# Kernel optimization log

Measured on AMD Instinct MI355X. Metric: run time of the kernel, lower is better.

Reference implementation:

```python
import jax, jax.numpy as jnp
import numpy as np

B, L, D, F = 4096, 200, 64, 100000


def setup_inputs() -> dict:
    key = jax.random.key(0)
    ks = jax.random.split(key, 12)
    film_hist = jax.random.randint(ks[0], (B, L), 0, F)                 # padded rated-film indices
    ratings = jax.random.uniform(ks[1], (B, L), jnp.float32) * 4.5 + 0.5  # letterboxd-style 0.5..5
    lengths = jax.random.randint(ks[2], (B,), 1, L + 1)                 # ragged history lengths (>=1)
    film_indices = jax.random.randint(ks[3], (B,), 0, F)                # target films to score
    emb_table = jax.random.normal(ks[4], (F, D), jnp.float32) * 0.1
    W1 = jax.random.normal(ks[5], (5 * D, 2 * D), jnp.float32) * 0.05
    b1 = jnp.zeros((2 * D,), jnp.float32)
    W2 = jax.random.normal(ks[6], (2 * D, D), jnp.float32) * 0.05
    b2 = jnp.zeros((D,), jnp.float32)
    W3 = jax.random.normal(ks[7], (D, 1), jnp.float32) * 0.05
    b3 = jnp.zeros((1,), jnp.float32)
    return {"film_hist": film_hist, "ratings": ratings, "lengths": lengths,
            "film_indices": film_indices, "emb_table": emb_table,
            "W1": W1, "b1": b1, "W2": W2, "b2": b2, "W3": W3, "b3": b3}


def _user_embeddings(film_hist, ratings, lengths, emb_table):
    # mask[b, l] = l < lengths[b]
    mask = jnp.arange(L)[None, :] < lengths[:, None]          # [B, L]
    n = lengths.astype(jnp.float32)                           # [B]
    mean_r = jnp.sum(jnp.where(mask, ratings, 0.0), axis=1) / n
    weights = ratings - mean_r[:, None] + 0.1                 # [B, L]
    hist_emb = emb_table[film_hist]                           # [B, L, D]
    w = hist_emb * weights[:, :, None]                        # weighted film embeddings
    m3 = mask[:, :, None]
    wmin = jnp.min(jnp.where(m3, w, jnp.inf), axis=1)
    wmax = jnp.max(jnp.where(m3, w, -jnp.inf), axis=1)
    wmean = jnp.sum(jnp.where(m3, w, 0.0), axis=1) / n[:, None]
    # median: sort valid entries (pads go to +inf at the end); torch.median
    # returns the lower middle element -> index (n-1)//2
    ws = jnp.sort(jnp.where(m3, w, jnp.inf), axis=1)
    mid = ((lengths - 1) // 2)[:, None, None]                 # [B,1,1]
    wmed = jnp.take_along_axis(ws, jnp.broadcast_to(mid, (B, 1, D)), axis=1)[:, 0, :]
    ue = jnp.concatenate([wmin, wmax, wmean, wmed], axis=1)   # [B, 4D]
    return ue / jnp.linalg.norm(ue, axis=1, keepdims=True)


def reference(film_hist, ratings, lengths, film_indices, emb_table, W1, b1, W2, b2, W3, b3):
    ue = _user_embeddings(film_hist, ratings, lengths, emb_table)  # [B, 4D]
    fe = emb_table[film_indices]                                   # [B, D]
    x = jnp.concatenate([ue, fe], axis=1)                          # [B, 5D]
    h = jax.nn.relu(x @ W1 + b1)   # Dropout(0.2) is identity in eval
    h = jax.nn.relu(h @ W2 + b2)
    return jax.nn.sigmoid(h @ W3 + b3)[:, 0]                       # [B]
```

## Files before the change

### kernel.cpp

```cpp
#include <hip/hip_runtime.h>
#include <hip/hip_bf16.h>
#include <stdint.h>


#define B_ 4096
#define L_ 200
#define D_ 64

__global__ __launch_bounds__(256) void stats_kernel(
    const int* __restrict__ film_hist,
    const float* __restrict__ ratings,
    const int* __restrict__ lengths,
    const int* __restrict__ film_indices,
    const float* __restrict__ emb,
    float* __restrict__ x)
{
  __shared__ uint2 pair_s[4][L_];

  const int t = threadIdx.x;
  const int wv = t >> 6;
  const int lane = t & 63;
  const int b = blockIdx.x * 4 + wv;
  const int n = lengths[b];

  const int fi = film_indices[b];
  const float fev = emb[(size_t)fi * D_ + lane];

  const int*   hp = film_hist + (size_t)b * L_;
  const float* rp = ratings  + (size_t)b * L_;
  int hv[4]; float rv[4]; float rsum = 0.f;
  #pragma unroll
  for (int j = 0; j < 4; ++j) {
    const int l = lane + 64*j;
    const bool v = l < n;
    hv[j] = v ? hp[l] : 0;
    rv[j] = v ? rp[l] : 0.f;
    rsum += v ? rv[j] : 0.f;
  }
  #pragma unroll
  for (int off = 32; off; off >>= 1) rsum += __shfl_xor(rsum, off);
  const float mr1 = 0.1f - rsum / (float)n;

  uint2* ps = pair_s[wv];
  #pragma unroll
  for (int j = 0; j < 4; ++j) {
    const int l = lane + 64*j;
    if (l < n) {
      uint2 e; e.x = ((uint32_t)hv[j]) << 8;
      e.y = __float_as_uint(rv[j] + mr1);
      ps[l] = e;
    }
  }

  float vmin = __builtin_inff(), vmax = -__builtin_inff(), vsum = 0.f;
  uint32_t PL[7][16];
  const char* eb = (const char*)emb;
  const uint32_t lane4 = (uint32_t)lane * 4u;

  #pragma unroll
  for (int c = 0; c < 7; ++c) {
    if (n > 32*c) {
      uint32_t W[16];
      #pragma unroll
      for (int p = 0; p < 16; ++p) {
        const int i0 = 32*c + 2*p, i1 = i0 + 1;
        const int l0 = (i0 < n) ? i0 : (n-1);
        const int l1 = (i1 < n) ? i1 : (n-1);
        const uint2 e0 = ps[l0];
        const uint2 e1 = ps[l1];
        const float w0 = *(const float*)(eb + (e0.x + lane4)) * __uint_as_float(e0.y);
        const float w1 = *(const float*)(eb + (e1.x + lane4)) * __uint_as_float(e1.y);
        vmin = fminf(vmin, fminf(w0, w1));
        vmax = fmaxf(vmax, fmaxf(w0, w1));
        vsum += (i0 < n) ? w0 : 0.f;
        vsum += (i1 < n) ? w1 : 0.f;
        const uint32_t u0 = __float_as_uint(w0);
        const uint32_t u1 = __float_as_uint(w1);
        const uint32_t k0 = u0 ^ (0x80000000u | (uint32_t)((int32_t)u0 >> 31));
        const uint32_t k1 = u1 ^ (0x80000000u | (uint32_t)((int32_t)u1 >> 31));
        W[p] = (k0 >> 16) | (k1 & 0xFFFF0000u);
      }
      #define XS(k, jj, m) { uint32_t tt = ((W[k] ^ (W[(k)|(jj)] >> (jj))) & (m)); \
                             W[k] ^= tt; W[(k)|(jj)] ^= (tt << (jj)); }
      XS(0,8,0x00FF00FFu) XS(1,8,0x00FF00FFu) XS(2,8,0x00FF00FFu) XS(3,8,0x00FF00FFu)
      XS(4,8,0x00FF00FFu) XS(5,8,0x00FF00FFu) XS(6,8,0x00FF00FFu) XS(7,8,0x00FF00FFu)
      XS(0,4,0x0F0F0F0Fu) XS(1,4,0x0F0F0F0Fu) XS(2,4,0x0F0F0F0Fu) XS(3,4,0x0F0F0F0Fu)
      XS(8,4,0x0F0F0F0Fu) XS(9,4,0x0F0F0F0Fu) XS(10,4,0x0F0F0F0Fu) XS(11,4,0x0F0F0F0Fu)
      XS(0,2,0x33333333u) XS(1,2,0x33333333u) XS(4,2,0x33333333u) XS(5,2,0x33333333u)
      XS(8,2,0x33333333u) XS(9,2,0x33333333u) XS(12,2,0x33333333u) XS(13,2,0x33333333u)
      XS(0,1,0x55555555u) XS(2,1,0x55555555u) XS(4,1,0x55555555u) XS(6,1,0x55555555u)
      XS(8,1,0x55555555u) XS(10,1,0x55555555u) XS(12,1,0x55555555u) XS(14,1,0x55555555u)
      #undef XS
      #pragma unroll
      for (int j = 0; j < 16; ++j) PL[c][j] = W[j];
    } else {
      #pragma unroll
      for (int j = 0; j < 16; ++j) PL[c][j] = 0u;
    }
  }

  uint32_t alive[7];
  #pragma unroll
  for (int c = 0; c < 7; ++c) {
    int v = n - 32*c; v = (v < 0) ? 0 : (v > 32 ? 32 : v);
    const int ce = (v + 1) >> 1, cf = v >> 1;
    uint32_t a = ((1u << ce) - 1u) << (16 - ce);
    if (cf) a |= ((1u << cf) - 1u) << (32 - cf);
    alive[c] = a;
  }

  int k = (n - 1) >> 1;
  int na = n;
  uint32_t prefix = 0;
  #pragma unroll
  for (int bb = 15; bb >= 0; --bb) {
    uint32_t t1[7];
    int cnt1 = 0;
    #pragma unroll
    for (int c = 0; c < 7; ++c) {
      t1[c] = alive[c] & PL[c][15 - bb];
      cnt1 += __popc(t1[c]);
    }
    const int cnt0 = na - cnt1;
    const bool zs = (k < cnt0);
    #pragma unroll
    for (int c = 0; c < 7; ++c)
      alive[c] = zs ? (alive[c] ^ t1[c]) : t1[c];
    na = zs ? cnt0 : cnt1;
    k  = zs ? k : (k - cnt0);
    prefix = zs ? prefix : (prefix | (1u << bb));
  }

  uint32_t key32 = (prefix << 16) | 0x8000u;
  const float med = (prefix & 0x8000u) ? __uint_as_float(key32 ^ 0x80000000u)
                                       : __uint_as_float(~key32);
  const float mean = vsum / (float)n;

  float ss = vmin*vmin + vmax*vmax + mean*mean + med*med;
  #pragma unroll
  for (int off = 32; off; off >>= 1) ss += __shfl_xor(ss, off);
  const float rn = 1.0f / sqrtf(ss);

  float* xb = x + (size_t)b * 320;
  xb[lane]        = vmin * rn;
  xb[64  + lane]  = vmax * rn;
  xb[128 + lane]  = mean * rn;
  xb[192 + lane]  = med  * rn;
  xb[256 + lane]  = fev;
}

#define U_ 4

__global__ __launch_bounds__(256) void mlp_kernel(
    const float* __restrict__ x,
    const float* __restrict__ W1, const float* __restrict__ b1,
    const float* __restrict__ W2, const float* __restrict__ b2,
    const float* __restrict__ W3, const float* __restrict__ b3,
    float* __restrict__ out)
{
  __shared__ float xs[U_*320];
  __shared__ float h1s[U_*128];
  __shared__ float h2s[U_*64];
  const int t = threadIdx.x;
  const int u0 = blockIdx.x * U_;

  for (int i = t; i < U_*80; i += 256)
    ((float4*)xs)[i] = ((const float4*)(x + (size_t)u0*320))[i];
  __syncthreads();

  {
    const int j = t & 127, g = t >> 7;
    const int ub = g*2;
    float acc[2];
    const float bj = b1[j];
    acc[0] = bj; acc[1] = bj;
    for (int i = 0; i < 320; i += 4) {
      float w0 = W1[(i+0)*128 + j];
      float w1 = W1[(i+1)*128 + j];
      float w2 = W1[(i+2)*128 + j];
      float w3 = W1[(i+3)*128 + j];
      #pragma unroll
      for (int q = 0; q < 2; ++q) {
        float4 xv = *(const float4*)&xs[(ub+q)*320 + i];
        acc[q] += xv.x*w0 + xv.y*w1 + xv.z*w2 + xv.w*w3;
      }
    }
    #pragma unroll
    for (int q = 0; q < 2; ++q) h1s[(ub+q)*128 + j] = fmaxf(acc[q], 0.f);
  }
  __syncthreads();

  {
    const int j = t & 63, g = t >> 6;
    float acc = b2[j];
    for (int i = 0; i < 128; i += 4) {
      float w0 = W2[(i+0)*64 + j];
      float w1 = W2[(i+1)*64 + j];
      float w2 = W2[(i+2)*64 + j];
      float w3 = W2[(i+3)*64 + j];
      float4 hv = *(const float4*)&h1s[g*128 + i];
      acc += hv.x*w0 + hv.y*w1 + hv.z*w2 + hv.w*w3;
    }
    h2s[g*64 + j] = fmaxf(acc, 0.f);
  }
  __syncthreads();

  if (t < U_*4) {
    const int u = t >> 2, sub = t & 3;
    float a = 0.f;
    #pragma unroll
    for (int i = 0; i < 16; ++i) a += h2s[u*64 + sub*16 + i] * W3[sub*16 + i];
    a += __shfl_xor(a, 1);
    a += __shfl_xor(a, 2);
    if (sub == 0) out[u0 + u] = 1.f / (1.f + __expf(-(a + b3[0])));
  }
}

extern "C" void kernel_launch(void* const* d_in, const int* in_sizes, int n_in,
                              void* d_out, int out_size, void* d_ws, size_t ws_size,
                              hipStream_t stream) {
  const int*   film_hist = (const int*)d_in[0];
  const float* ratings   = (const float*)d_in[1];
  const int*   lengths   = (const int*)d_in[2];
  const int*   film_idx  = (const int*)d_in[3];
  const float* emb       = (const float*)d_in[4];
  const float* W1 = (const float*)d_in[5];
  const float* b1 = (const float*)d_in[6];
  const float* W2 = (const float*)d_in[7];
  const float* b2 = (const float*)d_in[8];
  const float* W3 = (const float*)d_in[9];
  const float* b3 = (const float*)d_in[10];

  float* xbuf = (float*)d_ws;
  float* outp = (float*)d_out;

  stats_kernel<<<B_/4, 256, 0, stream>>>(film_hist, ratings, lengths, film_idx, emb, xbuf);
  mlp_kernel<<<B_/U_, 256, 0, stream>>>(xbuf, W1, b1, W2, b2, W3, b3, outp);
}
```

Measured before the change: 63.03 us.

## Drop LDS staging, defer sort-key transform, specialize median select by chunk count

Removes the shared-memory staging of (index, weight) pairs, so each lane now reads history indices and ratings straight from global memory (broadcast loads) inside the gather loop. The float-to-sortable-key transform moves from per-element work to a single bit-plane fixup after the transpose: the sign plane is inverted and the other planes are XORed with it. The median radix-select is templated on the number of active 32-element chunks and dispatched through a switch, so short histories skip the popcounts for empty chunks. A fast path for full chunks also avoids the per-element mask on the sum. The cost is more scalar or global loads per element and extra code size from seven template instantiations.

```diff
diff --git a/kernel.cpp b/kernel.cpp
--- a/kernel.cpp
+++ b/kernel.cpp
@@ -6,6 +6,34 @@
 #define B_ 4096
 #define L_ 200
 #define D_ 64
+
+template<int NC>
+__device__ __forceinline__ uint32_t select_kth(
+    const uint32_t (&PL)[7][16], const uint32_t (&alive0)[7], int k)
+{
+  uint32_t alive[NC];
+  int na = 0;
+  #pragma unroll
+  for (int c = 0; c < NC; ++c) { alive[c] = alive0[c]; na += __popc(alive[c]); }
+  uint32_t prefix = 0;
+  #pragma unroll
+  for (int bb = 15; bb >= 0; --bb) {
+    uint32_t t1[NC]; int cnt1 = 0;
+    #pragma unroll
+    for (int c = 0; c < NC; ++c) {
+      t1[c] = alive[c] & PL[c][15 - bb];
+      cnt1 += __popc(t1[c]);
+    }
+    const int cnt0 = na - cnt1;
+    const bool zs = (k < cnt0);
+    #pragma unroll
+    for (int c = 0; c < NC; ++c) alive[c] = zs ? (alive[c] ^ t1[c]) : t1[c];
+    na = zs ? cnt0 : cnt1;
+    k  = zs ? k : (k - cnt0);
+    prefix = zs ? prefix : (prefix | (1u << bb));
+  }
+  return prefix;
+}
 
 __global__ __launch_bounds__(256) void stats_kernel(
     const int* __restrict__ film_hist,
@@ -15,8 +43,6 @@
     const float* __restrict__ emb,
     float* __restrict__ x)
 {
-  __shared__ uint2 pair_s[4][L_];
-
   const int t = threadIdx.x;
   const int wv = t >> 6;
   const int lane = t & 63;
@@ -28,57 +54,44 @@
 
   const int*   hp = film_hist + (size_t)b * L_;
   const float* rp = ratings  + (size_t)b * L_;
-  int hv[4]; float rv[4]; float rsum = 0.f;
+
+  float rsum = 0.f;
   #pragma unroll
   for (int j = 0; j < 4; ++j) {
     const int l = lane + 64*j;
-    const bool v = l < n;
-    hv[j] = v ? hp[l] : 0;
-    rv[j] = v ? rp[l] : 0.f;
-    rsum += v ? rv[j] : 0.f;
+    rsum += (l < n) ? rp[l] : 0.f;
   }
   #pragma unroll
   for (int off = 32; off; off >>= 1) rsum += __shfl_xor(rsum, off);
   const float mr1 = 0.1f - rsum / (float)n;
 
-  uint2* ps = pair_s[wv];
-  #pragma unroll
-  for (int j = 0; j < 4; ++j) {
-    const int l = lane + 64*j;
-    if (l < n) {
-      uint2 e; e.x = ((uint32_t)hv[j]) << 8;
-      e.y = __float_as_uint(rv[j] + mr1);
-      ps[l] = e;
-    }
-  }
-
   float vmin = __builtin_inff(), vmax = -__builtin_inff(), vsum = 0.f;
   uint32_t PL[7][16];
-  const char* eb = (const char*)emb;
-  const uint32_t lane4 = (uint32_t)lane * 4u;
 
   #pragma unroll
   for (int c = 0; c < 7; ++c) {
     if (n > 32*c) {
+      const bool full = (32*c + 32 <= n);
       uint32_t W[16];
       #pragma unroll
       for (int p = 0; p < 16; ++p) {
         const int i0 = 32*c + 2*p, i1 = i0 + 1;
         const int l0 = (i0 < n) ? i0 : (n-1);
         const int l1 = (i1 < n) ? i1 : (n-1);
-        const uint2 e0 = ps[l0];
-        const uint2 e1 = ps[l1];
-        const float w0 = *(const float*)(eb + (e0.x + lane4)) * __uint_as_float(e0.y);
-        const float w1 = *(const float*)(eb + (e1.x + lane4)) * __uint_as_float(e1.y);
-        vmin = fminf(vmin, fminf(w0, w1));
-        vmax = fmaxf(vmax, fmaxf(w0, w1));
-        vsum += (i0 < n) ? w0 : 0.f;
-        vsum += (i1 < n) ? w1 : 0.f;
-        const uint32_t u0 = __float_as_uint(w0);
-        const uint32_t u1 = __float_as_uint(w1);
-        const uint32_t k0 = u0 ^ (0x80000000u | (uint32_t)((int32_t)u0 >> 31));
-        const uint32_t k1 = u1 ^ (0x80000000u | (uint32_t)((int32_t)u1 >> 31));
-        W[p] = (k0 >> 16) | (k1 & 0xFFFF0000u);
+        const int h0 = hp[l0];
+        const int h1 = hp[l1];
+        const float r0 = rp[l0];
+        const float r1 = rp[l1];
+        const float* e0 = emb + (size_t)h0 * D_;
+        const float* e1 = emb + (size_t)h1 * D_;
+        const float w0 = e0[lane] * (r0 + mr1);
+        const float w1 = e1[lane] * (r1 + mr1);
+        vmin = fminf(fminf(vmin, w0), w1);
+        vmax = fmaxf(fmaxf(vmax, w0), w1);
+        if (full) vsum += w0 + w1;
+        else { vsum += (i0 < n) ? w0 : 0.f; vsum += (i1 < n) ? w1 : 0.f; }
+        W[p] = __builtin_amdgcn_perm(__float_as_uint(w1), __float_as_uint(w0),
+                                     0x07060302u);
       }
       #define XS(k, jj, m) { uint32_t tt = ((W[k] ^ (W[(k)|(jj)] >> (jj))) & (m)); \
                              W[k] ^= tt; W[(k)|(jj)] ^= (tt << (jj)); }
@@ -91,6 +104,12 @@
       XS(0,1,0x55555555u) XS(2,1,0x55555555u) XS(4,1,0x55555555u) XS(6,1,0x55555555u)
       XS(8,1,0x55555555u) XS(10,1,0x55555555u) XS(12,1,0x55555555u) XS(14,1,0x55555555u)
       #undef XS
+      {
+        const uint32_t S = W[0];
+        W[0] = ~S;
+        #pragma unroll
+        for (int j = 1; j < 16; ++j) W[j] ^= S;
+      }
       #pragma unroll
       for (int j = 0; j < 16; ++j) PL[c][j] = W[j];
     } else {
@@ -109,26 +128,17 @@
     alive[c] = a;
   }
 
-  int k = (n - 1) >> 1;
-  int na = n;
-  uint32_t prefix = 0;
-  #pragma unroll
-  for (int bb = 15; bb >= 0; --bb) {
-    uint32_t t1[7];
-    int cnt1 = 0;
-    #pragma unroll
-    for (int c = 0; c < 7; ++c) {
-      t1[c] = alive[c] & PL[c][15 - bb];
-      cnt1 += __popc(t1[c]);
-    }
-    const int cnt0 = na - cnt1;
-    const bool zs = (k < cnt0);
-    #pragma unroll
-    for (int c = 0; c < 7; ++c)
-      alive[c] = zs ? (alive[c] ^ t1[c]) : t1[c];
-    na = zs ? cnt0 : cnt1;
-    k  = zs ? k : (k - cnt0);
-    prefix = zs ? prefix : (prefix | (1u << bb));
+  const int k = (n - 1) >> 1;
+  const int nct = (n + 31) >> 5;
+  uint32_t prefix;
+  switch (nct) {
+    case 1: prefix = select_kth<1>(PL, alive, k); break;
+    case 2: prefix = select_kth<2>(PL, alive, k); break;
+    case 3: prefix = select_kth<3>(PL, alive, k); break;
+    case 4: prefix = select_kth<4>(PL, alive, k); break;
+    case 5: prefix = select_kth<5>(PL, alive, k); break;
+    case 6: prefix = select_kth<6>(PL, alive, k); break;
+    default: prefix = select_kth<7>(PL, alive, k); break;
   }
 
   uint32_t key32 = (prefix << 16) | 0x8000u;
```

Result: slower. 155.9 us (+147.3%).
